# Performance work log

Measured on AMD Instinct MI355X. Metric: run time of the kernel, lower is better.

## Reference

```python
import jax, jax.numpy as jnp
import numpy as np

# S4D diagonal SSM kernel generation (disc='zoh', real_type='exp', no state, rate=1.0)
H = 768      # model width (number of SSM copies)
N = 64       # state size per SSM
CH = 1       # kernel channels
NSSM = 768   # n_ssm == H -> repeat = 1 (untied)
L_VAL = 2048 # target kernel length


def setup_inputs() -> dict:
    key = jax.random.key(0)
    k_dt, k_C = jax.random.split(key, 2)
    # dt log-uniform in [1e-3, 1e-1]
    log_dt = np.log(1e-3) + jax.random.uniform(k_dt, (H,), dtype=jnp.float32) * (np.log(1e-1) - np.log(1e-3))
    # B = 1 + 0j  (standard S4D init), stored as real/imag pair
    B_ri = jnp.concatenate([jnp.ones((NSSM, N, 1), jnp.float32), jnp.zeros((NSSM, N, 1), jnp.float32)], axis=-1)
    # A = -0.5 + i*pi*n  (S4D-Lin); real_type='exp' -> inv_A_real = log(-A_real) = log(0.5)
    inv_A_real = jnp.full((NSSM, N), np.log(0.5), dtype=jnp.float32)
    A_imag = jnp.tile(np.pi * jnp.arange(N, dtype=jnp.float32)[None, :], (NSSM, 1))
    C_ri = jax.random.normal(k_C, (CH, H, N, 2), dtype=jnp.float32)
    return {"log_dt": log_dt, "B_ri": B_ri, "inv_A_real": inv_A_real,
            "A_imag": A_imag, "C_ri": C_ri, "L": L_VAL}


def reference(log_dt, B_ri, inv_A_real, A_imag, C_ri, L):
    dt = jnp.exp(log_dt)                               # (H,)
    A = -jnp.exp(inv_A_real) + 1j * A_imag             # (n_ssm, N) complex
    rep = H // A.shape[0]
    A = jnp.tile(A, (rep, 1))                          # (H, N)
    B = B_ri[..., 0] + 1j * B_ri[..., 1]               # (n_ssm, N)
    B = jnp.tile(B, (rep, 1))[None]                    # (1, H, N)
    C = C_ri[..., 0] + 1j * C_ri[..., 1]               # (CH, H, N)
    C = (B[:, None, :, :] * C).reshape(-1, H, N)       # (CH, H, N)
    dtA = A * dt[:, None]                              # (H, N)
    # ZOH discretization of C
    C = C * (jnp.exp(dtA) - 1.0) / A                   # (CH, H, N)
    # log-Vandermonde: K[c,h,l] = 2*Re( sum_n C[c,h,n] * exp(dtA[h,n] * l) )
    ell = jnp.arange(L, dtype=jnp.float32)
    V = jnp.exp(dtA[:, :, None] * ell)                 # (H, N, L) complex64 -- dominant intermediate
    K = 2.0 * jnp.einsum('chn,hnl->chl', C, V).real    # (CH, H, L)
    return K.astype(jnp.float32)
```

## Files before the change

### kernel.cpp

```cpp
#include <hip/hip_runtime.h>
#include <math.h>


typedef float v2f __attribute__((ext_vector_type(2)));

#define H_DIM 768
#define N_DIM 64
#define L_DIM 2048
#define TPB   256
#define LTH   64
#define LCH   32

__global__ __launch_bounds__(TPB, 3) void s4d_gen_kernel(
    const float* __restrict__ log_dt,
    const float* __restrict__ B_ri,
    const float* __restrict__ inv_A_real,
    const float* __restrict__ A_imag,
    const float* __restrict__ C_ri,
    float* __restrict__ out)
{
    __shared__ float4 sP0[N_DIM];
    __shared__ float4 sP1[N_DIM];
    __shared__ v2f    sC1p[N_DIM / 2];
    __shared__ v2f    sNC2p[N_DIM / 2];
    __shared__ float  sRed[2][LCH][LTH];

    const int h  = blockIdx.x;
    const int t  = threadIdx.x;
    const int nb = t >> 6;
    const int tl = t & 63;

    if (t < N_DIM) {
        const int n   = t;
        const int idx = h * N_DIM + n;
        const float dt = expf(log_dt[h]);
        const float Ar = -expf(inv_A_real[idx]);
        const float Ai = A_imag[idx];
        const float dtAr = Ar * dt;
        const float dtAi = Ai * dt;
        const float e  = expf(dtAr);
        float s, c;
        sincosf(dtAi, &s, &c);
        const float wr = e * c, wi = e * s;
        const float inv = 1.0f / (Ar * Ar + Ai * Ai);
        const float nr = wr - 1.0f, ni = wi;
        const float qr = (nr * Ar + ni * Ai) * inv;
        const float qi = (ni * Ar - nr * Ai) * inv;
        const float Br = B_ri[2 * idx], Bi = B_ri[2 * idx + 1];
        const float Cr = C_ri[2 * idx], Ci = C_ri[2 * idx + 1];
        const float BCr = Br * Cr - Bi * Ci;
        const float BCi = Br * Ci + Bi * Cr;
        const float Gr = 2.0f * (BCr * qr - BCi * qi);
        const float Gi = 2.0f * (BCr * qi + BCi * qr);
        const double revs32 = (double)dtAi * (32.0 / (2.0 * M_PI));
        const float  r32f   = (float)(revs32 - floor(revs32));
        const float  l2m32  = dtAr * (32.0f * 1.4426950408889634f);
        sP0[n] = make_float4(r32f, l2m32, Gr, Gi);
        sP1[n] = make_float4(Gr * wr - Gi * wi, Gr * wi + Gi * wr, 0.0f, 0.0f);
        ((float*)sC1p)[n]  = 2.0f * wr;
        ((float*)sNC2p)[n] = -(wr * wr + wi * wi);
    }
    __syncthreads();

    v2f acc2[LCH];
    #pragma unroll
    for (int j = 0; j < LCH; ++j) acc2[j] = (v2f){0.0f, 0.0f};

    const int   nbase = nb * 16;
    const float tlf   = (float)tl;

    #pragma unroll 1
    for (int pp = 0; pp < 4; ++pp) {
        const int na = nbase + 4 * pp;
        const int nc = na + 2;

        const float4 pA0 = sP0[na], pA1 = sP0[na + 1];
        const float4 pB0 = sP0[nc], pB1 = sP0[nc + 1];
        const float4 qA0 = sP1[na], qA1 = sP1[na + 1];
        const float4 qB0 = sP1[nc], qB1 = sP1[nc + 1];

        const float fA0 = __builtin_amdgcn_fractf(pA0.x * tlf);
        const float fA1 = __builtin_amdgcn_fractf(pA1.x * tlf);
        const float fB0 = __builtin_amdgcn_fractf(pB0.x * tlf);
        const float fB1 = __builtin_amdgcn_fractf(pB1.x * tlf);
        const float snA0 = __builtin_amdgcn_sinf(fA0), csA0 = __builtin_amdgcn_cosf(fA0);
        const float snA1 = __builtin_amdgcn_sinf(fA1), csA1 = __builtin_amdgcn_cosf(fA1);
        const float snB0 = __builtin_amdgcn_sinf(fB0), csB0 = __builtin_amdgcn_cosf(fB0);
        const float snB1 = __builtin_amdgcn_sinf(fB1), csB1 = __builtin_amdgcn_cosf(fB1);
        const float mA0 = __builtin_amdgcn_exp2f(pA0.y * tlf);
        const float mA1 = __builtin_amdgcn_exp2f(pA1.y * tlf);
        const float mB0 = __builtin_amdgcn_exp2f(pB0.y * tlf);
        const float mB1 = __builtin_amdgcn_exp2f(pB1.y * tlf);
        const float urA0 = mA0 * csA0, uiA0 = mA0 * snA0;
        const float urA1 = mA1 * csA1, uiA1 = mA1 * snA1;
        const float urB0 = mB0 * csB0, uiB0 = mB0 * snB0;
        const float urB1 = mB1 * csB1, uiB1 = mB1 * snB1;

        v2f s0A = (v2f){fmaf(pA0.z, urA0, -(pA0.w * uiA0)),
                        fmaf(pA1.z, urA1, -(pA1.w * uiA1))};
        v2f s1A = (v2f){fmaf(qA0.x, urA0, -(qA0.y * uiA0)),
                        fmaf(qA1.x, urA1, -(qA1.y * uiA1))};
        v2f s0B = (v2f){fmaf(pB0.z, urB0, -(pB0.w * uiB0)),
                        fmaf(pB1.z, urB1, -(pB1.w * uiB1))};
        v2f s1B = (v2f){fmaf(qB0.x, urB0, -(qB0.y * uiB0)),
                        fmaf(qB1.x, urB1, -(qB1.y * uiB1))};

        const v2f c1A  = sC1p[na >> 1],  c1B  = sC1p[nc >> 1];
        const v2f nc2A = sNC2p[na >> 1], nc2B = sNC2p[nc >> 1];

        #pragma unroll
        for (int j = 0; j < LCH; ++j) {
            acc2[j] += s0A;
            acc2[j] += s0B;
            v2f tA = c1A * s1A;
            v2f nA = __builtin_elementwise_fma(nc2A, s0A, tA);
            s0A = s1A; s1A = nA;
            v2f tB = c1B * s1B;
            v2f nB = __builtin_elementwise_fma(nc2B, s0B, tB);
            s0B = s1B; s1B = nB;
        }
    }

    float acc[LCH];
    #pragma unroll
    for (int j = 0; j < LCH; ++j) acc[j] = acc2[j].x + acc2[j].y;

    if (nb >= 2) {
        #pragma unroll
        for (int j = 0; j < LCH; ++j) sRed[nb - 2][j][tl] = acc[j];
    }
    __syncthreads();
    if (nb < 2) {
        #pragma unroll
        for (int j = 0; j < LCH; ++j) acc[j] += sRed[nb][j][tl];
    }
    __syncthreads();
    if (nb == 1) {
        #pragma unroll
        for (int j = 0; j < LCH; ++j) sRed[0][j][tl] = acc[j];
    }
    __syncthreads();
    if (nb == 0) {
        #pragma unroll
        for (int j = 0; j < LCH; ++j) acc[j] += sRed[0][j][tl];
        float* op = out + (size_t)h * L_DIM + tl * LCH;
        #pragma unroll
        for (int j = 0; j < LCH; j += 4) {
            *reinterpret_cast<float4*>(op + j) =
                make_float4(acc[j], acc[j + 1], acc[j + 2], acc[j + 3]);
        }
    }
}

extern "C" void kernel_launch(void* const* d_in, const int* in_sizes, int n_in,
                              void* d_out, int out_size, void* d_ws, size_t ws_size,
                              hipStream_t stream) {
    const float* log_dt     = (const float*)d_in[0];
    const float* B_ri       = (const float*)d_in[1];
    const float* inv_A_real = (const float*)d_in[2];
    const float* A_imag     = (const float*)d_in[3];
    const float* C_ri       = (const float*)d_in[4];
    float* out = (float*)d_out;
    hipLaunchKernelGGL(s4d_gen_kernel, dim3(H_DIM), dim3(TPB), 0, stream,
                       log_dt, B_ri, inv_A_real, A_imag, C_ri, out);
}
```

Measured before the change: 72.87 us.

## Widen recurrence to eight modes per pass and flatten block reduction

```diff
diff --git a/kernel.cpp b/kernel.cpp
--- a/kernel.cpp
+++ b/kernel.cpp
@@ -21,9 +21,7 @@
 {
     __shared__ float4 sP0[N_DIM];
     __shared__ float4 sP1[N_DIM];
-    __shared__ v2f    sC1p[N_DIM / 2];
-    __shared__ v2f    sNC2p[N_DIM / 2];
-    __shared__ float  sRed[2][LCH][LTH];
+    __shared__ v2f    sRedV[3][LCH][LTH];
 
     const int h  = blockIdx.x;
     const int t  = threadIdx.x;
@@ -56,9 +54,8 @@
         const float  r32f   = (float)(revs32 - floor(revs32));
         const float  l2m32  = dtAr * (32.0f * 1.4426950408889634f);
         sP0[n] = make_float4(r32f, l2m32, Gr, Gi);
-        sP1[n] = make_float4(Gr * wr - Gi * wi, Gr * wi + Gi * wr, 0.0f, 0.0f);
-        ((float*)sC1p)[n]  = 2.0f * wr;
-        ((float*)sNC2p)[n] = -(wr * wr + wi * wi);
+        sP1[n] = make_float4(Gr * wr - Gi * wi, Gr * wi + Gi * wr,
+                             2.0f * wr, -(wr * wr + wi * wi));
     }
     __syncthreads();
 
@@ -69,80 +66,65 @@
     const int   nbase = nb * 16;
     const float tlf   = (float)tl;
 
-    #pragma unroll 1
-    for (int pp = 0; pp < 4; ++pp) {
-        const int na = nbase + 4 * pp;
-        const int nc = na + 2;
+    #pragma unroll
+    for (int half = 0; half < 2; ++half) {
+        const int n0 = nbase + half * 8;
 
-        const float4 pA0 = sP0[na], pA1 = sP0[na + 1];
-        const float4 pB0 = sP0[nc], pB1 = sP0[nc + 1];
-        const float4 qA0 = sP1[na], qA1 = sP1[na + 1];
-        const float4 qB0 = sP1[nc], qB1 = sP1[nc + 1];
-
-        const float fA0 = __builtin_amdgcn_fractf(pA0.x * tlf);
-        const float fA1 = __builtin_amdgcn_fractf(pA1.x * tlf);
-        const float fB0 = __builtin_amdgcn_fractf(pB0.x * tlf);
-        const float fB1 = __builtin_amdgcn_fractf(pB1.x * tlf);
-        const float snA0 = __builtin_amdgcn_sinf(fA0), csA0 = __builtin_amdgcn_cosf(fA0);
-        const float snA1 = __builtin_amdgcn_sinf(fA1), csA1 = __builtin_amdgcn_cosf(fA1);
-        const float snB0 = __builtin_amdgcn_sinf(fB0), csB0 = __builtin_amdgcn_cosf(fB0);
-        const float snB1 = __builtin_amdgcn_sinf(fB1), csB1 = __builtin_amdgcn_cosf(fB1);
-        const float mA0 = __builtin_amdgcn_exp2f(pA0.y * tlf);
-        const float mA1 = __builtin_amdgcn_exp2f(pA1.y * tlf);
-        const float mB0 = __builtin_amdgcn_exp2f(pB0.y * tlf);
-        const float mB1 = __builtin_amdgcn_exp2f(pB1.y * tlf);
-        const float urA0 = mA0 * csA0, uiA0 = mA0 * snA0;
-        const float urA1 = mA1 * csA1, uiA1 = mA1 * snA1;
-        const float urB0 = mB0 * csB0, uiB0 = mB0 * snB0;
-        const float urB1 = mB1 * csB1, uiB1 = mB1 * snB1;
-
-        v2f s0A = (v2f){fmaf(pA0.z, urA0, -(pA0.w * uiA0)),
-                        fmaf(pA1.z, urA1, -(pA1.w * uiA1))};
-        v2f s1A = (v2f){fmaf(qA0.x, urA0, -(qA0.y * uiA0)),
-                        fmaf(qA1.x, urA1, -(qA1.y * uiA1))};
-        v2f s0B = (v2f){fmaf(pB0.z, urB0, -(pB0.w * uiB0)),
-                        fmaf(pB1.z, urB1, -(pB1.w * uiB1))};
-        v2f s1B = (v2f){fmaf(qB0.x, urB0, -(qB0.y * uiB0)),
-                        fmaf(qB1.x, urB1, -(qB1.y * uiB1))};
-
-        const v2f c1A  = sC1p[na >> 1],  c1B  = sC1p[nc >> 1];
-        const v2f nc2A = sNC2p[na >> 1], nc2B = sNC2p[nc >> 1];
+        float s0s[8], s1s[8], c1s[8], nc2s[8];
+        #pragma unroll
+        for (int k = 0; k < 8; ++k) {
+            const float4 p = sP0[n0 + k];
+            const float4 q = sP1[n0 + k];
+            const float f  = __builtin_amdgcn_fractf(p.x * tlf);
+            const float m  = __builtin_amdgcn_exp2f(p.y * tlf);
+            const float cs = __builtin_amdgcn_cosf(f);
+            const float sn = __builtin_amdgcn_sinf(f);
+            const float ur = m * cs, ui = m * sn;
+            s0s[k]  = fmaf(p.z, ur, -(p.w * ui));
+            s1s[k]  = fmaf(q.x, ur, -(q.y * ui));
+            c1s[k]  = q.z;
+            nc2s[k] = q.w;
+        }
+        v2f S0[4], S1[4], C1[4], NC2[4];
+        #pragma unroll
+        for (int k = 0; k < 4; ++k) {
+            S0[k]  = (v2f){s0s[2*k],  s0s[2*k+1]};
+            S1[k]  = (v2f){s1s[2*k],  s1s[2*k+1]};
+            C1[k]  = (v2f){c1s[2*k],  c1s[2*k+1]};
+            NC2[k] = (v2f){nc2s[2*k], nc2s[2*k+1]};
+        }
 
         #pragma unroll
         for (int j = 0; j < LCH; ++j) {
-            acc2[j] += s0A;
-            acc2[j] += s0B;
-            v2f tA = c1A * s1A;
-            v2f nA = __builtin_elementwise_fma(nc2A, s0A, tA);
-            s0A = s1A; s1A = nA;
-            v2f tB = c1B * s1B;
-            v2f nB = __builtin_elementwise_fma(nc2B, s0B, tB);
-            s0B = s1B; s1B = nB;
+            const v2f t1 = S0[0] + S0[1];
+            const v2f t2 = S0[2] + S0[3];
+            acc2[j] += t1;
+            acc2[j] += t2;
+            #pragma unroll
+            for (int k = 0; k < 4; ++k) {
+                v2f tt = C1[k] * S1[k];
+                v2f nn = __builtin_elementwise_fma(NC2[k], S0[k], tt);
+                S0[k] = S1[k]; S1[k] = nn;
+            }
         }
     }
 
-    float acc[LCH];
-    #pragma unroll
-    for (int j = 0; j < LCH; ++j) acc[j] = acc2[j].x + acc2[j].y;
-
-    if (nb >= 2) {
+    if (nb != 0) {
         #pragma unroll
-        for (int j = 0; j < LCH; ++j) sRed[nb - 2][j][tl] = acc[j];
-    }
-    __syncthreads();
-    if (nb < 2) {
-        #pragma unroll
-        for (int j = 0; j < LCH; ++j) acc[j] += sRed[nb][j][tl];
-    }
-    __syncthreads();
-    if (nb == 1) {
-        #pragma unroll
-        for (int j = 0; j < LCH; ++j) sRed[0][j][tl] = acc[j];
+        for (int j = 0; j < LCH; ++j) sRedV[nb - 1][j][tl] = acc2[j];
     }
     __syncthreads();
     if (nb == 0) {
         #pragma unroll
-        for (int j = 0; j < LCH; ++j) acc[j] += sRed[0][j][tl];
+        for (int j = 0; j < LCH; ++j) {
+            const v2f a = sRedV[0][j][tl];
+            const v2f b = sRedV[1][j][tl];
+            const v2f c = sRedV[2][j][tl];
+            acc2[j] += a + b + c;
+        }
+        float acc[LCH];
+        #pragma unroll
+        for (int j = 0; j < LCH; ++j) acc[j] = acc2[j].x + acc2[j].y;
         float* op = out + (size_t)h * L_DIM + tl * LCH;
         #pragma unroll
         for (int j = 0; j < LCH; j += 4) {
```

Measured after the change: 73.74 us. No clear change (+1.2%).
